# Kernel optimization log

Hardware: AMD Instinct MI355X
Metric: run time of the kernel (lower is better)

The kernel has to match this reference:

```python
import jax, jax.numpy as jnp
import numpy as np

N_NODES = 50000
N_EDGES = 800000
NUM_FEATURES = 128
H1, H2, H3 = 256, 512, 256


def setup_inputs() -> dict:
    key = jax.random.key(0)
    ks = jax.random.split(key, 14)

    def lin(kw, fan_in, fan_out):
        # torch nn.Linear-style init, stored as [in, out] for x @ W
        bound = 1.0 / np.sqrt(fan_in)
        W = jax.random.uniform(kw, (fan_in, fan_out), jnp.float32, -bound, bound)
        b = jnp.zeros((fan_out,), jnp.float32)
        return W, b

    x = jax.random.normal(ks[0], (N_NODES, NUM_FEATURES), jnp.float32)
    edge_index = jax.random.randint(ks[1], (2, N_EDGES), 0, N_NODES, jnp.int64 if jax.config.jax_enable_x64 else jnp.int32)

    W1, b1 = lin(ks[2], NUM_FEATURES, H1)
    W2, b2 = lin(ks[3], H1, H2)
    W3, b3 = lin(ks[4], H2, H3)
    Wf1, bf1 = lin(ks[5], H3, 128)
    Wf2, bf2 = lin(ks[6], 128, 64)
    Wf3, bf3 = lin(ks[7], 64, 1)

    return {"x": x, "edge_index": edge_index,
            "W1": W1, "b1": b1, "W2": W2, "b2": b2, "W3": W3, "b3": b3,
            "Wf1": Wf1, "bf1": bf1, "Wf2": Wf2, "bf2": bf2, "Wf3": Wf3, "bf3": bf3}


def gcn_conv(x, W, b, row, col, dinv_row_col, n):
    # PyG GCNConv: out = D^{-1/2} (A+I) D^{-1/2} (x W) + b, self-loops already in row/col
    h = x @ W                              # [N, out]
    msg = h[row] * dinv_row_col[:, None]   # gather + edge-wise scale: [E+N, out]
    return jax.ops.segment_sum(msg, col, num_segments=n) + b


def reference(x, edge_index, W1, b1, W2, b2, W3, b3, Wf1, bf1, Wf2, bf2, Wf3, bf3):
    n = x.shape[0]
    loop = jnp.arange(n, dtype=edge_index.dtype)
    row = jnp.concatenate([edge_index[0], loop])   # sources (with self-loops)
    col = jnp.concatenate([edge_index[1], loop])   # targets (with self-loops)

    # symmetric normalization (computed once; identical for all three convs)
    deg = jax.ops.segment_sum(jnp.ones(col.shape[0], x.dtype), col, num_segments=n)
    dinv = jnp.where(deg > 0, jax.lax.rsqrt(deg), 0.0)
    norm = dinv[row] * dinv[col]                   # [E+N]

    h = jax.nn.relu(gcn_conv(x, W1, b1, row, col, norm, n))
    h = jax.nn.relu(gcn_conv(h, W2, b2, row, col, norm, n))
    h = jax.nn.relu(gcn_conv(h, W3, b3, row, col, norm, n))

    g = jnp.mean(h, axis=0, keepdims=True)         # [1, H3]
    g = jax.nn.relu(g @ Wf1 + bf1)
    g = jax.nn.relu(g @ Wf2 + bf2)
    return g @ Wf3 + bf3                           # [1, 1]
```

## Files before the change

kernel.cpp:

```cpp
#include <hip/hip_runtime.h>
#include <hip/hip_bf16.h>

#define N_NODES 50000
#define N_EDGES 800000
#define N_BUCKETS 64
#define M_PAD 50048
#define SCAN_NB 196

typedef short short8 __attribute__((ext_vector_type(8)));
typedef float floatx4 __attribute__((ext_vector_type(4)));
typedef float floatx2 __attribute__((ext_vector_type(2)));

__device__ __forceinline__ unsigned short f2bf(float f) {
    unsigned u = __float_as_uint(f);
    unsigned r = (u + 0x7fff + ((u >> 16) & 1)) >> 16;
    return (unsigned short)r;
}
__device__ __forceinline__ float bf2f(unsigned short h) {
    return __uint_as_float(((unsigned)h) << 16);
}
__device__ __forceinline__ void expand2(unsigned u, float& lo, float& hi) {
    lo = __uint_as_float(u << 16);
    hi = __uint_as_float(u & 0xffff0000u);
}

__device__ __forceinline__ unsigned pack4_fp8(float f0, float f1, float f2, float f3) {
    int v = __builtin_amdgcn_cvt_pk_fp8_f32(f0, f1, 0, false);
    v = __builtin_amdgcn_cvt_pk_fp8_f32(f2, f3, v, true);
    return (unsigned)v;
}
__device__ __forceinline__ void accum_fp8x4(float* a, unsigned u, float w) {
    floatx2 lo = __builtin_amdgcn_cvt_pk_f32_fp8((int)u, false);
    floatx2 hi = __builtin_amdgcn_cvt_pk_f32_fp8((int)u, true);
    a[0] += lo[0] * w; a[1] += lo[1] * w;
    a[2] += hi[0] * w; a[3] += hi[1] * w;
}
__device__ __forceinline__ void accum_fp8x2(float* a, unsigned u, float w) {
    floatx2 lo = __builtin_amdgcn_cvt_pk_f32_fp8((int)u, false);
    a[0] += lo[0] * w; a[1] += lo[1] * w;
}

__device__ __forceinline__ void gload16(const void* gp, void* lp) {
    __builtin_amdgcn_global_load_lds(
        (const __attribute__((address_space(1))) unsigned int*)gp,
        (__attribute__((address_space(3))) unsigned int*)lp,
        16, 0, 0);
}

__global__ void k_init(int* __restrict__ cnt, float* __restrict__ gb) {
    int i = blockIdx.x * blockDim.x + threadIdx.x;
    if (i < N_NODES) cnt[i] = 0;
    if (i < N_BUCKETS * 256) gb[i] = 0.0f;
}

__global__ void k_count(const int* __restrict__ col, int* __restrict__ cnt) {
    int e = blockIdx.x * blockDim.x + threadIdx.x;
    if (e < N_EDGES) atomicAdd(&cnt[col[e]], 1);
}

__global__ __launch_bounds__(256) void k_scanA(const int* __restrict__ cnt,
                                               int* __restrict__ bsum) {
    __shared__ int red[256];
    int t = threadIdx.x;
    int i = blockIdx.x * 256 + t;
    red[t] = (i < N_NODES) ? ((cnt[i] + 1) & ~1) : 0;
    __syncthreads();
    for (int d = 128; d > 0; d >>= 1) {
        if (t < d) red[t] += red[t + d];
        __syncthreads();
    }
    if (t == 0) bsum[blockIdx.x] = red[0];
}

__global__ __launch_bounds__(256) void k_scanB(const int* __restrict__ bsum,
                                               int* __restrict__ bbase,
                                               int* __restrict__ off) {
    __shared__ int sc[256];
    int t = threadIdx.x;
    sc[t] = (t < SCAN_NB) ? bsum[t] : 0;
    __syncthreads();
    for (int d = 1; d < 256; d <<= 1) {
        int v = 0;
        if (t >= d) v = sc[t - d];
        __syncthreads();
        if (t >= d) sc[t] += v;
        __syncthreads();
    }
    if (t < SCAN_NB) bbase[t] = sc[t] - bsum[t];
    if (t == SCAN_NB - 1) off[N_NODES] = sc[t];
}

__global__ __launch_bounds__(256) void k_scanC(const int* __restrict__ cnt,
                                               const int* __restrict__ bbase,
                                               int* __restrict__ off,
                                               int* __restrict__ cursor,
                                               float* __restrict__ dinv,
                                               int2* __restrict__ epack) {
    __shared__ int sc[256];
    int t = threadIdx.x;
    int i = blockIdx.x * 256 + t;
    int c = (i < N_NODES) ? cnt[i] : 0;
    int cap = (c + 1) & ~1;
    sc[t] = cap;
    __syncthreads();
    for (int d = 1; d < 256; d <<= 1) {
        int v = 0;
        if (t >= d) v = sc[t - d];
        __syncthreads();
        if (t >= d) sc[t] += v;
        __syncthreads();
    }
    if (i < N_NODES) {
        int excl = sc[t] - cap + bbase[blockIdx.x];
        off[i] = excl;
        cursor[i] = excl;
        dinv[i] = 1.0f / sqrtf((float)(c + 1));
        if (c & 1) epack[excl + c] = make_int2(i, 0);
    }
}

__global__ void k_fill(const int* __restrict__ row, const int* __restrict__ col,
                       const float* __restrict__ dinv, int* __restrict__ cursor,
                       int2* __restrict__ epack) {
    int e = blockIdx.x * blockDim.x + threadIdx.x;
    if (e >= N_EDGES) return;
    int v = col[e];
    int p = atomicAdd(&cursor[v], 1);
    int r = row[e];
    epack[p] = make_int2(r, __float_as_int(dinv[r]));
}

__global__ void k_prepW(const float* __restrict__ W,
                        unsigned short* __restrict__ Th,
                        unsigned short* __restrict__ Tl, int K, int N) {
    int idx = blockIdx.x * blockDim.x + threadIdx.x;
    if (idx >= K * N) return;
    int n = idx / K, k = idx - n * K;
    float v = W[(size_t)k * N + n];
    unsigned short h = f2bf(v);
    Th[idx] = h;
    Tl[idx] = f2bf(v - bf2f(h));
}

__global__ void k_prepX8(const float* __restrict__ x, unsigned char* __restrict__ xq) {
    int i = blockIdx.x * blockDim.x + threadIdx.x;
    if (i >= N_NODES * 32) return;
    const float* s = x + (size_t)i * 4;
    *(unsigned*)&xq[(size_t)i * 4] = pack4_fp8(s[0], s[1], s[2], s[3]);
}

template <int DIM, int POOL>
__global__ __launch_bounds__(256) void k_aggf(
    const unsigned char* __restrict__ xq, const int* __restrict__ off,
    const int2* __restrict__ epack, const float* __restrict__ dinv,
    const float* __restrict__ bias, unsigned short* __restrict__ outb,
    float* __restrict__ gb) {
    const int FPL = DIM / 64;
    __shared__ float gpart[256];
    if (POOL) {
        gpart[threadIdx.x] = 0.0f;
        __syncthreads();
    }
    int wv = threadIdx.x >> 6;
    int li = threadIdx.x & 63;
    int v = blockIdx.x * 4 + wv;
    int f = li * FPL;
    float dv = dinv[v];
    const unsigned char* __restrict__ xf = xq + f;
    float a0[FPL], a1[FPL], a2[FPL], a3[FPL];
#pragma unroll
    for (int i = 0; i < FPL; ++i) { a0[i] = 0.f; a1[i] = 0.f; a2[i] = 0.f; a3[i] = 0.f; }
    if (FPL == 4) {
        accum_fp8x4(a0, *(const unsigned*)&xf[(size_t)v * DIM], dv);
    } else {
        accum_fp8x2(a0, (unsigned)*(const unsigned short*)&xf[(size_t)v * DIM], dv);
    }
    int s = off[v], e = off[v + 1];
    int j = s;
    for (; j + 4 <= e; j += 4) {
        int4 d0 = *(const int4*)&epack[j];
        int4 d1 = *(const int4*)&epack[j + 2];
        if (FPL == 4) {
            unsigned g0 = *(const unsigned*)&xf[(size_t)d0.x * DIM];
            unsigned g1 = *(const unsigned*)&xf[(size_t)d0.z * DIM];
            unsigned g2 = *(const unsigned*)&xf[(size_t)d1.x * DIM];
            unsigned g3 = *(const unsigned*)&xf[(size_t)d1.z * DIM];
            accum_fp8x4(a0, g0, __int_as_float(d0.y));
            accum_fp8x4(a1, g1, __int_as_float(d0.w));
            accum_fp8x4(a2, g2, __int_as_float(d1.y));
            accum_fp8x4(a3, g3, __int_as_float(d1.w));
        } else {
            unsigned g0 = *(const unsigned short*)&xf[(size_t)d0.x * DIM];
            unsigned g1 = *(const unsigned short*)&xf[(size_t)d0.z * DIM];
            unsigned g2 = *(const unsigned short*)&xf[(size_t)d1.x * DIM];
            unsigned g3 = *(const unsigned short*)&xf[(size_t)d1.z * DIM];
            accum_fp8x2(a0, g0, __int_as_float(d0.y));
            accum_fp8x2(a1, g1, __int_as_float(d0.w));
            accum_fp8x2(a2, g2, __int_as_float(d1.y));
            accum_fp8x2(a3, g3, __int_as_float(d1.w));
        }
    }
    if (j < e) {
        int4 d0 = *(const int4*)&epack[j];
        if (FPL == 4) {
            unsigned g0 = *(const unsigned*)&xf[(size_t)d0.x * DIM];
            unsigned g1 = *(const unsigned*)&xf[(size_t)d0.z * DIM];
            accum_fp8x4(a0, g0, __int_as_float(d0.y));
            accum_fp8x4(a1, g1, __int_as_float(d0.w));
        } else {
            unsigned g0 = *(const unsigned short*)&xf[(size_t)d0.x * DIM];
            unsigned g1 = *(const unsigned short*)&xf[(size_t)d0.z * DIM];
            accum_fp8x2(a0, g0, __int_as_float(d0.y));
            accum_fp8x2(a1, g1, __int_as_float(d0.w));
        }
    }
    float acc[FPL];
#pragma unroll
    for (int i = 0; i < FPL; ++i)
        acc[i] = ((a0[i] + a1[i]) + (a2[i] + a3[i])) * dv;
    if (!POOL) {
        if (FPL == 4) {
            uint2 o;
            o.x = (unsigned)f2bf(acc[0]) | ((unsigned)f2bf(acc[1]) << 16);
            o.y = (unsigned)f2bf(acc[2]) | ((unsigned)f2bf(acc[3]) << 16);
            *(uint2*)&outb[(size_t)v * DIM + f] = o;
        } else {
            unsigned o = (unsigned)f2bf(acc[0]) | ((unsigned)f2bf(acc[1]) << 16);
            *(unsigned*)&outb[(size_t)v * DIM + f] = o;
        }
    } else {
#pragma unroll
        for (int i = 0; i < FPL; ++i) {
            float r = fmaxf(acc[i] + bias[f + i], 0.0f);
            atomicAdd(&gpart[f + i], r);
        }
        __syncthreads();
        atomicAdd(&gb[(blockIdx.x & (N_BUCKETS - 1)) * 256 + threadIdx.x],
                  gpart[threadIdx.x]);
    }
}

template <int BIAS, int RELU, int OUTFP8>
__global__ __launch_bounds__(256) void k_gemm_b(
    const unsigned short* __restrict__ A,
    const unsigned short* __restrict__ Bh, const unsigned short* __restrict__ Bl,
    const float* __restrict__ bias, void* __restrict__ Cout,
    int M, int K, int N) {
    __shared__ unsigned short smem[4 * 4096];
    unsigned short* As  = smem;
    unsigned short* BsH = smem + 4096;
    unsigned short* BsL = smem + 8192;
    int tid = threadIdx.x;
    int lane = tid & 63;
    int w = tid >> 6;
    int wr = w & 1, wc = w >> 1;
    int bm = blockIdx.x * 128, bn = blockIdx.y * 128;

    floatx4 acc[4][4];
    floatx4 zero = {0.f, 0.f, 0.f, 0.f};
#pragma unroll
    for (int t = 0; t < 4; ++t)
#pragma unroll
        for (int u = 0; u < 4; ++u) acc[t][u] = zero;

    int c0 = w * 2, c1 = c0 + 1;
    int srow = lane >> 2;
    int kg = ((lane & 3) - ((lane >> 3) & 3)) & 3;
    int kc = kg * 8;
    const unsigned short* Ap0 = A + (size_t)(bm + c0 * 16 + srow) * K + kc;
    const unsigned short* Ap1 = A + (size_t)(bm + c1 * 16 + srow) * K + kc;
    const unsigned short* Bh0 = Bh + (size_t)(bn + c0 * 16 + srow) * K + kc;
    const unsigned short* Bh1 = Bh + (size_t)(bn + c1 * 16 + srow) * K + kc;
    const unsigned short* Bl0 = Bl + (size_t)(bn + c0 * 16 + srow) * K + kc;
    const unsigned short* Bl1 = Bl + (size_t)(bn + c1 * 16 + srow) * K + kc;

    const int KT = K >> 5;
    int fr = lane & 15;
    int fq = lane >> 4;
    int cl = ((fq + (fr >> 1)) & 3) * 8;

    for (int kt = 0; kt < KT; ++kt) {
        int k0 = kt * 32;
        gload16(Ap0 + k0, As + c0 * 512);
        gload16(Ap1 + k0, As + c1 * 512);
        gload16(Bh0 + k0, BsH + c0 * 512);
        gload16(Bh1 + k0, BsH + c1 * 512);
        gload16(Bl0 + k0, BsL + c0 * 512);
        gload16(Bl1 + k0, BsL + c1 * 512);
        __syncthreads();
        short8 av[4], bhv[4], blv[4];
#pragma unroll
        for (int t = 0; t < 4; ++t) {
            av[t]  = *(const short8*)&As[(wr * 64 + t * 16 + fr) * 32 + cl];
            bhv[t] = *(const short8*)&BsH[(wc * 64 + t * 16 + fr) * 32 + cl];
            blv[t] = *(const short8*)&BsL[(wc * 64 + t * 16 + fr) * 32 + cl];
        }
#pragma unroll
        for (int t = 0; t < 4; ++t)
#pragma unroll
            for (int u = 0; u < 4; ++u) {
                acc[t][u] = __builtin_amdgcn_mfma_f32_16x16x32_bf16(av[t], bhv[u], acc[t][u], 0, 0, 0);
                acc[t][u] = __builtin_amdgcn_mfma_f32_16x16x32_bf16(av[t], blv[u], acc[t][u], 0, 0, 0);
            }
        __syncthreads();
    }

    unsigned short* cq = smem + w * 4096;
#pragma unroll
    for (int u = 0; u < 4; ++u) {
        int colq = u * 16 + fr;
        float bv = BIAS ? bias[bn + wc * 64 + colq] : 0.0f;
#pragma unroll
        for (int t = 0; t < 4; ++t) {
#pragma unroll
            for (int r = 0; r < 4; ++r) {
                float o = acc[t][u][r] + bv;
                if (RELU) o = fmaxf(o, 0.f);
                cq[(t * 16 + fq * 4 + r) * 64 + colq] = f2bf(o);
            }
        }
    }
    __syncthreads();
    int lr = tid >> 4;
    int lc = (tid & 15) * 8;
    int wcq = lc >> 6;
    int lcq = lc & 63;
#pragma unroll
    for (int i = 0; i < 8; ++i) {
        int rowt = i * 16 + lr;
        int wrq = rowt >> 6;
        const unsigned short* src =
            smem + (wrq + wcq * 2) * 4096 + (rowt & 63) * 64 + lcq;
        int rowg = bm + rowt;
        if (rowg < M) {
            if (!OUTFP8) {
                unsigned short* C = (unsigned short*)Cout;
                *(uint4*)&C[(size_t)rowg * N + bn + lc] = *(const uint4*)src;
            } else {
                uint4 b = *(const uint4*)src;
                float f0, f1, f2, f3, f4, f5, f6, f7;
                expand2(b.x, f0, f1); expand2(b.y, f2, f3);
                expand2(b.z, f4, f5); expand2(b.w, f6, f7);
                uint2 q;
                q.x = pack4_fp8(f0, f1, f2, f3);
                q.y = pack4_fp8(f4, f5, f6, f7);
                unsigned char* C8 = (unsigned char*)Cout;
                *(uint2*)&C8[(size_t)rowg * N + bn + lc] = q;
            }
        }
    }
}

__global__ void k_mlp(const float* __restrict__ gb,
                      const float* __restrict__ Wf1, const float* __restrict__ bf1,
                      const float* __restrict__ Wf2, const float* __restrict__ bf2,
                      const float* __restrict__ Wf3, const float* __restrict__ bf3,
                      float* __restrict__ out) {
    __shared__ float s0[256], s1[128], s2[64];
    int t = threadIdx.x;
    float sum = 0.0f;
    for (int b = 0; b < N_BUCKETS; ++b) sum += gb[b * 256 + t];
    s0[t] = sum * (1.0f / (float)N_NODES);
    __syncthreads();
    if (t < 128) {
        float a = bf1[t];
        for (int k = 0; k < 256; ++k) a += s0[k] * Wf1[k * 128 + t];
        s1[t] = fmaxf(a, 0.0f);
    }
    __syncthreads();
    if (t < 64) {
        float a = bf2[t];
        for (int k = 0; k < 128; ++k) a += s1[k] * Wf2[k * 64 + t];
        s2[t] = fmaxf(a, 0.0f);
    }
    __syncthreads();
    if (t == 0) {
        float a = bf3[0];
        for (int k = 0; k < 64; ++k) a += s2[k] * Wf3[k];
        out[0] = a;
    }
}

extern "C" void kernel_launch(void* const* d_in, const int* in_sizes, int n_in,
                              void* d_out, int out_size, void* d_ws, size_t ws_size,
                              hipStream_t stream) {
    const float* x  = (const float*)d_in[0];
    const int* ei   = (const int*)d_in[1];
    const float* W1 = (const float*)d_in[2];
    const float* b1 = (const float*)d_in[3];
    const float* W2 = (const float*)d_in[4];
    const float* b2 = (const float*)d_in[5];
    const float* W3 = (const float*)d_in[6];
    const float* b3 = (const float*)d_in[7];
    const float* Wf1 = (const float*)d_in[8];
    const float* bf1 = (const float*)d_in[9];
    const float* Wf2 = (const float*)d_in[10];
    const float* bf2 = (const float*)d_in[11];
    const float* Wf3 = (const float*)d_in[12];
    const float* bf3 = (const float*)d_in[13];
    float* out = (float*)d_out;

    char* p = (char*)d_ws;
    auto alloc = [&](size_t bytes) {
        void* r = (void*)p;
        p += (bytes + 255) & ~((size_t)255);
        return r;
    };
    int*   cnt    = (int*)  alloc(N_NODES * sizeof(int));
    int*   off    = (int*)  alloc((N_NODES + 1) * sizeof(int));
    int*   cursor = (int*)  alloc(N_NODES * sizeof(int));
    int*   bsum   = (int*)  alloc(SCAN_NB * sizeof(int));
    int*   bbase  = (int*)  alloc(SCAN_NB * sizeof(int));
    float* dinv   = (float*)alloc(N_NODES * sizeof(float));
    int2*  epack  = (int2*) alloc((size_t)(N_EDGES + N_NODES) * sizeof(int2));
    float* gb     = (float*)alloc(N_BUCKETS * 256 * sizeof(float));
    unsigned short* W1h = (unsigned short*)alloc(128 * 256 * 2);
    unsigned short* W1l = (unsigned short*)alloc(128 * 256 * 2);
    unsigned short* W2h = (unsigned short*)alloc(256 * 512 * 2);
    unsigned short* W2l = (unsigned short*)alloc(256 * 512 * 2);
    unsigned short* W3h = (unsigned short*)alloc(512 * 256 * 2);
    unsigned short* W3l = (unsigned short*)alloc(512 * 256 * 2);
    unsigned char*  xq  = (unsigned char*) alloc((size_t)N_NODES * 128);
    unsigned short* t0  = (unsigned short*)alloc((size_t)M_PAD * 128 * 2);
    unsigned char*  h1q = (unsigned char*) alloc((size_t)N_NODES * 256);
    unsigned short* t1  = (unsigned short*)alloc((size_t)M_PAD * 256 * 2);
    unsigned short* h2  = (unsigned short*)alloc((size_t)M_PAD * 512 * 2);
    unsigned char*  t2q = (unsigned char*) alloc((size_t)N_NODES * 256);

    const int* row = ei;
    const int* col = ei + N_EDGES;

    const int NB = (N_NODES + 255) / 256;
    const int EB = (N_EDGES + 255) / 256;

    k_init<<<NB, 256, 0, stream>>>(cnt, gb);
    k_count<<<EB, 256, 0, stream>>>(col, cnt);
    k_scanA<<<SCAN_NB, 256, 0, stream>>>(cnt, bsum);
    k_scanB<<<1, 256, 0, stream>>>(bsum, bbase, off);
    k_scanC<<<SCAN_NB, 256, 0, stream>>>(cnt, bbase, off, cursor, dinv, epack);
    k_fill<<<EB, 256, 0, stream>>>(row, col, dinv, cursor, epack);

    k_prepW<<<(128 * 256 + 255) / 256, 256, 0, stream>>>(W1, W1h, W1l, 128, 256);
    k_prepW<<<(256 * 512 + 255) / 256, 256, 0, stream>>>(W2, W2h, W2l, 256, 512);
    k_prepW<<<(512 * 256 + 255) / 256, 256, 0, stream>>>(W3, W3h, W3l, 512, 256);
    k_prepX8<<<(N_NODES * 32 + 255) / 256, 256, 0, stream>>>(x, xq);

    const int M = N_NODES;
    const int MB = (M + 127) / 128;

    k_aggf<128, 0><<<N_NODES / 4, 256, 0, stream>>>(
        xq, off, epack, dinv, nullptr, t0, nullptr);
    {
        dim3 grid(MB, 256 / 128);
        k_gemm_b<1, 1, 1><<<grid, 256, 0, stream>>>(t0, W1h, W1l, b1, h1q, M, 128, 256);
    }
    k_aggf<256, 0><<<N_NODES / 4, 256, 0, stream>>>(
        h1q, off, epack, dinv, nullptr, t1, nullptr);
    {
        dim3 grid(MB, 512 / 128);
        k_gemm_b<1, 1, 0><<<grid, 256, 0, stream>>>(t1, W2h, W2l, b2, h2, M, 256, 512);
    }
    {
        dim3 grid(MB, 256 / 128);
        k_gemm_b<0, 0, 1><<<grid, 256, 0, stream>>>(h2, W3h, W3l, nullptr, t2q, M, 512, 256);
    }
    k_aggf<256, 1><<<N_NODES / 4, 256, 0, stream>>>(
        t2q, off, epack, dinv, b3, nullptr, gb);

    k_mlp<<<1, 256, 0, stream>>>(gb, Wf1, bf1, Wf2, bf2, Wf3, bf3, out);
}
```

Baseline: 456.0 us.

## Fold source-side dinv into producers and shrink edge list to int indices

Source-node normalization dinv[r] is now applied when features are produced (in the fp8 quantization of x and in the GEMM epilogues), so the aggregation kernels only sum gathered rows and apply the target dinv at the end. The edge list drops the per-edge weight and becomes a plain int array padded to multiples of 4, with pad slots pointing at a zeroed dummy row. The aggregation loop is unrolled by 8. This cuts edge-list bandwidth and per-edge multiplies, at the cost of extra padding gathers and quantizing pre-scaled values to fp8, which changes rounding.

```diff
diff --git a/kernel.cpp b/kernel.cpp
--- a/kernel.cpp
+++ b/kernel.cpp
@@ -6,6 +6,7 @@
 #define N_BUCKETS 64
 #define M_PAD 50048
 #define SCAN_NB 196
+#define ZROW N_NODES
 
 typedef short short8 __attribute__((ext_vector_type(8)));
 typedef float floatx4 __attribute__((ext_vector_type(4)));
@@ -29,15 +30,15 @@
     v = __builtin_amdgcn_cvt_pk_fp8_f32(f2, f3, v, true);
     return (unsigned)v;
 }
-__device__ __forceinline__ void accum_fp8x4(float* a, unsigned u, float w) {
+__device__ __forceinline__ void acc4(float* a, unsigned u) {
     floatx2 lo = __builtin_amdgcn_cvt_pk_f32_fp8((int)u, false);
     floatx2 hi = __builtin_amdgcn_cvt_pk_f32_fp8((int)u, true);
-    a[0] += lo[0] * w; a[1] += lo[1] * w;
-    a[2] += hi[0] * w; a[3] += hi[1] * w;
-}
-__device__ __forceinline__ void accum_fp8x2(float* a, unsigned u, float w) {
+    a[0] += lo[0]; a[1] += lo[1];
+    a[2] += hi[0]; a[3] += hi[1];
+}
+__device__ __forceinline__ void acc2(float* a, unsigned u) {
     floatx2 lo = __builtin_amdgcn_cvt_pk_f32_fp8((int)u, false);
-    a[0] += lo[0] * w; a[1] += lo[1] * w;
+    a[0] += lo[0]; a[1] += lo[1];
 }
 
 __device__ __forceinline__ void gload16(const void* gp, void* lp) {
@@ -47,10 +48,19 @@
         16, 0, 0);
 }
 
-__global__ void k_init(int* __restrict__ cnt, float* __restrict__ gb) {
+__global__ void k_init(int* __restrict__ cnt, float* __restrict__ gb,
+                       unsigned char* __restrict__ xq,
+                       unsigned char* __restrict__ h1q,
+                       unsigned char* __restrict__ t2q) {
     int i = blockIdx.x * blockDim.x + threadIdx.x;
     if (i < N_NODES) cnt[i] = 0;
     if (i < N_BUCKETS * 256) gb[i] = 0.0f;
+    if (blockIdx.x == 0) {
+        int t = threadIdx.x;
+        if (t < 32) ((unsigned*)(xq + (size_t)ZROW * 128))[t] = 0u;
+        if (t < 64) ((unsigned*)(h1q + (size_t)ZROW * 256))[t] = 0u;
+        if (t < 64) ((unsigned*)(t2q + (size_t)ZROW * 256))[t] = 0u;
+    }
 }
 
 __global__ void k_count(const int* __restrict__ col, int* __restrict__ cnt) {
@@ -63,7 +73,7 @@
     __shared__ int red[256];
     int t = threadIdx.x;
     int i = blockIdx.x * 256 + t;
-    red[t] = (i < N_NODES) ? ((cnt[i] + 1) & ~1) : 0;
+    red[t] = (i < N_NODES) ? ((cnt[i] + 4) & ~3) : 0;
     __syncthreads();
     for (int d = 128; d > 0; d >>= 1) {
         if (t < d) red[t] += red[t + d];
@@ -95,12 +105,12 @@
                                                int* __restrict__ off,
                                                int* __restrict__ cursor,
                                                float* __restrict__ dinv,
-                                               int2* __restrict__ epack) {
+                                               int* __restrict__ esrc) {
     __shared__ int sc[256];
     int t = threadIdx.x;
     int i = blockIdx.x * 256 + t;
     int c = (i < N_NODES) ? cnt[i] : 0;
-    int cap = (c + 1) & ~1;
+    int cap = (c + 4) & ~3;
     sc[t] = cap;
     __syncthreads();
     for (int d = 1; d < 256; d <<= 1) {
@@ -115,19 +125,17 @@
         off[i] = excl;
         cursor[i] = excl;
         dinv[i] = 1.0f / sqrtf((float)(c + 1));
-        if (c & 1) epack[excl + c] = make_int2(i, 0);
+        esrc[excl + c] = i;
+        for (int p = c + 1; p < cap; ++p) esrc[excl + p] = ZROW;
     }
 }
 
 __global__ void k_fill(const int* __restrict__ row, const int* __restrict__ col,
-                       const float* __restrict__ dinv, int* __restrict__ cursor,
-                       int2* __restrict__ epack) {
+                       int* __restrict__ cursor, int* __restrict__ esrc) {
     int e = blockIdx.x * blockDim.x + threadIdx.x;
     if (e >= N_EDGES) return;
-    int v = col[e];
-    int p = atomicAdd(&cursor[v], 1);
-    int r = row[e];
-    epack[p] = make_int2(r, __float_as_int(dinv[r]));
+    int p = atomicAdd(&cursor[col[e]], 1);
+    esrc[p] = row[e];
 }
 
 __global__ void k_prepW(const float* __restrict__ W,
@@ -142,22 +150,24 @@
     Tl[idx] = f2bf(v - bf2f(h));
 }
 
-__global__ void k_prepX8(const float* __restrict__ x, unsigned char* __restrict__ xq) {
+__global__ void k_prepX8(const float* __restrict__ x, const float* __restrict__ dinv,
+                         unsigned char* __restrict__ xq) {
     int i = blockIdx.x * blockDim.x + threadIdx.x;
     if (i >= N_NODES * 32) return;
+    float sc = dinv[i >> 5];
     const float* s = x + (size_t)i * 4;
-    *(unsigned*)&xq[(size_t)i * 4] = pack4_fp8(s[0], s[1], s[2], s[3]);
+    *(unsigned*)&xq[(size_t)i * 4] = pack4_fp8(s[0] * sc, s[1] * sc, s[2] * sc, s[3] * sc);
 }
 
 template <int DIM, int POOL>
-__global__ __launch_bounds__(256) void k_aggf(
+__global__ __launch_bounds__(256) void k_agg(
     const unsigned char* __restrict__ xq, const int* __restrict__ off,
-    const int2* __restrict__ epack, const float* __restrict__ dinv,
+    const int* __restrict__ esrc, const float* __restrict__ dinv,
     const float* __restrict__ bias, unsigned short* __restrict__ outb,
     float* __restrict__ gb) {
     const int FPL = DIM / 64;
     __shared__ float gpart[256];
-    if (POOL) {
+    if constexpr (POOL) {
         gpart[threadIdx.x] = 0.0f;
         __syncthreads();
     }
@@ -165,61 +175,59 @@
     int li = threadIdx.x & 63;
     int v = blockIdx.x * 4 + wv;
     int f = li * FPL;
-    float dv = dinv[v];
     const unsigned char* __restrict__ xf = xq + f;
     float a0[FPL], a1[FPL], a2[FPL], a3[FPL];
 #pragma unroll
     for (int i = 0; i < FPL; ++i) { a0[i] = 0.f; a1[i] = 0.f; a2[i] = 0.f; a3[i] = 0.f; }
-    if (FPL == 4) {
-        accum_fp8x4(a0, *(const unsigned*)&xf[(size_t)v * DIM], dv);
-    } else {
-        accum_fp8x2(a0, (unsigned)*(const unsigned short*)&xf[(size_t)v * DIM], dv);
-    }
-    int s = off[v], e = off[v + 1];
-    int j = s;
-    for (; j + 4 <= e; j += 4) {
-        int4 d0 = *(const int4*)&epack[j];
-        int4 d1 = *(const int4*)&epack[j + 2];
-        if (FPL == 4) {
-            unsigned g0 = *(const unsigned*)&xf[(size_t)d0.x * DIM];
-            unsigned g1 = *(const unsigned*)&xf[(size_t)d0.z * DIM];
-            unsigned g2 = *(const unsigned*)&xf[(size_t)d1.x * DIM];
-            unsigned g3 = *(const unsigned*)&xf[(size_t)d1.z * DIM];
-            accum_fp8x4(a0, g0, __int_as_float(d0.y));
-            accum_fp8x4(a1, g1, __int_as_float(d0.w));
-            accum_fp8x4(a2, g2, __int_as_float(d1.y));
-            accum_fp8x4(a3, g3, __int_as_float(d1.w));
+    int j = off[v], e = off[v + 1];
+    for (; j + 8 <= e; j += 8) {
+        int4 dA = *(const int4*)&esrc[j];
+        int4 dB = *(const int4*)&esrc[j + 4];
+        if constexpr (DIM == 256) {
+            unsigned g0 = *(const unsigned*)&xf[(size_t)dA.x * DIM];
+            unsigned g1 = *(const unsigned*)&xf[(size_t)dA.y * DIM];
+            unsigned g2 = *(const unsigned*)&xf[(size_t)dA.z * DIM];
+            unsigned g3 = *(const unsigned*)&xf[(size_t)dA.w * DIM];
+            unsigned g4 = *(const unsigned*)&xf[(size_t)dB.x * DIM];
+            unsigned g5 = *(const unsigned*)&xf[(size_t)dB.y * DIM];
+            unsigned g6 = *(const unsigned*)&xf[(size_t)dB.z * DIM];
+            unsigned g7 = *(const unsigned*)&xf[(size_t)dB.w * DIM];
+            acc4(a0, g0); acc4(a1, g1); acc4(a2, g2); acc4(a3, g3);
+            acc4(a0, g4); acc4(a1, g5); acc4(a2, g6); acc4(a3, g7);
         } else {
-            unsigned g0 = *(const unsigned short*)&xf[(size_t)d0.x * DIM];
-            unsigned g1 = *(const unsigned short*)&xf[(size_t)d0.z * DIM];
-            unsigned g2 = *(const unsigned short*)&xf[(size_t)d1.x * DIM];
-            unsigned g3 = *(const unsigned short*)&xf[(size_t)d1.z * DIM];
-            accum_fp8x2(a0, g0, __int_as_float(d0.y));
-            accum_fp8x2(a1, g1, __int_as_float(d0.w));
-            accum_fp8x2(a2, g2, __int_as_float(d1.y));
-            accum_fp8x2(a3, g3, __int_as_float(d1.w));
+            unsigned g0 = *(const unsigned short*)&xf[(size_t)dA.x * DIM];
+            unsigned g1 = *(const unsigned short*)&xf[(size_t)dA.y * DIM];
+            unsigned g2 = *(const unsigned short*)&xf[(size_t)dA.z * DIM];
+            unsigned g3 = *(const unsigned short*)&xf[(size_t)dA.w * DIM];
+            unsigned g4 = *(const unsigned short*)&xf[(size_t)dB.x * DIM];
+            unsigned g5 = *(const unsigned short*)&xf[(size_t)dB.y * DIM];
+            unsigned g6 = *(const unsigned short*)&xf[(size_t)dB.z * DIM];
+            unsigned g7 = *(const unsigned short*)&xf[(size_t)dB.w * DIM];
+            acc2(a0, g0); acc2(a1, g1); acc2(a2, g2); acc2(a3, g3);
+            acc2(a0, g4); acc2(a1, g5); acc2(a2, g6); acc2(a3, g7);
         }
     }
     if (j < e) {
-        int4 d0 = *(const int4*)&epack[j];
-        if (FPL == 4) {
-            unsigned g0 = *(const unsigned*)&xf[(size_t)d0.x * DIM];
-            unsigned g1 = *(const unsigned*)&xf[(size_t)d0.z * DIM];
-            accum_fp8x4(a0, g0, __int_as_float(d0.y));
-            accum_fp8x4(a1, g1, __int_as_float(d0.w));
+        int4 dA = *(const int4*)&esrc[j];
+        if constexpr (DIM == 256) {
+            acc4(a0, *(const unsigned*)&xf[(size_t)dA.x * DIM]);
+            acc4(a1, *(const unsigned*)&xf[(size_t)dA.y * DIM]);
+            acc4(a2, *(const unsigned*)&xf[(size_t)dA.z * DIM]);
+            acc4(a3, *(const unsigned*)&xf[(size_t)dA.w * DIM]);
         } else {
-            unsigned g0 = *(const unsigned short*)&xf[(size_t)d0.x * DIM];
-            unsigned g1 = *(const unsigned short*)&xf[(size_t)d0.z * DIM];
-            accum_fp8x2(a0, g0, __int_as_float(d0.y));
-            accum_fp8x2(a1, g1, __int_as_float(d0.w));
-        }
-    }
+            acc2(a0, *(const unsigned short*)&xf[(size_t)dA.x * DIM]);
+            acc2(a1, *(const unsigned short*)&xf[(size_t)dA.y * DIM]);
+            acc2(a2, *(const unsigned short*)&xf[(size_t)dA.z * DIM]);
+            acc2(a3, *(const unsigned short*)&xf[(size_t)dA.w * DIM]);
+        }
+    }
+    float dv = dinv[v];
     float acc[FPL];
 #pragma unroll
     for (int i = 0; i < FPL; ++i)
         acc[i] = ((a0[i] + a1[i]) + (a2[i] + a3[i])) * dv;
-    if (!POOL) {
-        if (FPL == 4) {
+    if constexpr (!POOL) {
+        if constexpr (DIM == 256) {
             uint2 o;
             o.x = (unsigned)f2bf(acc[0]) | ((unsigned)f2bf(acc[1]) << 16);
             o.y = (unsigned)f2bf(acc[2]) | ((unsigned)f2bf(acc[3]) << 16);
@@ -240,12 +248,12 @@
     }
 }
 
-template <int BIAS, int RELU, int OUTFP8>
+template <int BIAS, int RELU, int OUTFP8, int DVSCALE>
 __global__ __launch_bounds__(256) void k_gemm_b(
     const unsigned short* __restrict__ A,
     const unsigned short* __restrict__ Bh, const unsigned short* __restrict__ Bl,
-    const float* __restrict__ bias, void* __restrict__ Cout,
-    int M, int K, int N) {
+    const float* __restrict__ bias, const float* __restrict__ dinv,
+    void* __restrict__ Cout, int M, int K, int N) {
     __shared__ unsigned short smem[4 * 4096];
     unsigned short* As  = smem;
     unsigned short* BsH = smem + 4096;
@@ -337,13 +345,14 @@
                 unsigned short* C = (unsigned short*)Cout;
                 *(uint4*)&C[(size_t)rowg * N + bn + lc] = *(const uint4*)src;
             } else {
+                float sc = DVSCALE ? dinv[rowg] : 1.0f;
                 uint4 b = *(const uint4*)src;
                 float f0, f1, f2, f3, f4, f5, f6, f7;
                 expand2(b.x, f0, f1); expand2(b.y, f2, f3);
                 expand2(b.z, f4, f5); expand2(b.w, f6, f7);
                 uint2 q;
-                q.x = pack4_fp8(f0, f1, f2, f3);
-                q.y = pack4_fp8(f4, f5, f6, f7);
+                q.x = pack4_fp8(f0 * sc, f1 * sc, f2 * sc, f3 * sc);
+                q.y = pack4_fp8(f4 * sc, f5 * sc, f6 * sc, f7 * sc);
                 unsigned char* C8 = (unsigned char*)Cout;
                 *(uint2*)&C8[(size_t)rowg * N + bn + lc] = q;
             }
@@ -412,7 +421,7 @@
     int*   bsum   = (int*)  alloc(SCAN_NB * sizeof(int));
     int*   bbase  = (int*)  alloc(SCAN_NB * sizeof(int));
     float* dinv   = (float*)alloc(N_NODES * sizeof(float));
-    int2*  epack  = (int2*) alloc((size_t)(N_EDGES + N_NODES) * sizeof(int2));
+    int*   esrc   = (int*)  alloc((size_t)(N_EDGES + 4 * N_NODES) * sizeof(int));
     float* gb     = (float*)alloc(N_BUCKETS * 256 * sizeof(float));
     unsigned short* W1h = (unsigned short*)alloc(128 * 256 * 2);
     unsigned short* W1l = (unsigned short*)alloc(128 * 256 * 2);
@@ -420,12 +429,12 @@
     unsigned short* W2l = (unsigned short*)alloc(256 * 512 * 2);
     unsigned short* W3h = (unsigned short*)alloc(512 * 256 * 2);
     unsigned short* W3l = (unsigned short*)alloc(512 * 256 * 2);
-    unsigned char*  xq  = (unsigned char*) alloc((size_t)N_NODES * 128);
+    unsigned char*  xq  = (unsigned char*) alloc((size_t)(N_NODES + 1) * 128);
     unsigned short* t0  = (unsigned short*)alloc((size_t)M_PAD * 128 * 2);
-    unsigned char*  h1q = (unsigned char*) alloc((size_t)N_NODES * 256);
+    unsigned char*  h1q = (unsigned char*) alloc((size_t)(N_NODES + 1) * 256);
     unsigned short* t1  = (unsigned short*)alloc((size_t)M_PAD * 256 * 2);
     unsigned short* h2  = (unsigned short*)alloc((size_t)M_PAD * 512 * 2);
-    unsigned char*  t2q = (unsigned char*) alloc((size_t)N_NODES * 256);
+    unsigned char*  t2q = (unsigned char*) alloc((size_t)(N_NODES + 1) * 256);
 
     const int* row = ei;
     const int* col = ei + N_EDGES;
@@ -433,39 +442,39 @@
     const int NB = (N_NODES + 255) / 256;
     const int EB = (N_EDGES + 255) / 256;
 
-    k_init<<<NB, 256, 0, stream>>>(cnt, gb);
+    k_init<<<NB, 256, 0, stream>>>(cnt, gb, xq, h1q, t2q);
     k_count<<<EB, 256, 0, stream>>>(col, cnt);
     k_scanA<<<SCAN_NB, 256, 0, stream>>>(cnt, bsum);
     k_scanB<<<1, 256, 0, stream>>>(bsum, bbase, off);
-    k_scanC<<<SCAN_NB, 256, 0, stream>>>(cnt, bbase, off, cursor, dinv, epack);
-    k_fill<<<EB, 256, 0, stream>>>(row, col, dinv, cursor, epack);
+    k_scanC<<<SCAN_NB, 256, 0, stream>>>(cnt, bbase, off, cursor, dinv, esrc);
+    k_fill<<<EB, 256, 0, stream>>>(row, col, cursor, esrc);
 
     k_prepW<<<(128 * 256 + 255) / 256, 256, 0, stream>>>(W1, W1h, W1l, 128, 256);
     k_prepW<<<(256 * 512 + 255) / 256, 256, 0, stream>>>(W2, W2h, W2l, 256, 512);
     k_prepW<<<(512 * 256 + 255) / 256, 256, 0, stream>>>(W3, W3h, W3l, 512, 256);
-    k_prepX8<<<(N_NODES * 32 + 255) / 256, 256, 0, stream>>>(x, xq);
+    k_prepX8<<<(N_NODES * 32 + 255) / 256, 256, 0, stream>>>(x, dinv, xq);
 
     const int M = N_NODES;
     const int MB = (M + 127) / 128;
 
-    k_aggf<128, 0><<<N_NODES / 4, 256, 0, stream>>>(
-        xq, off, epack, dinv, nullptr, t0, nullptr);
+    k_agg<128, 0><<<N_NODES / 4, 256, 0, stream>>>(
+        xq, off, esrc, dinv, nullptr, t0, nullptr);
     {
         dim3 grid(MB, 256 / 128);
-        k_gemm_b<1, 1, 1><<<grid, 256, 0, stream>>>(t0, W1h, W1l, b1, h1q, M, 128, 256);
-    }
-    k_aggf<256, 0><<<N_NODES / 4, 256, 0, stream>>>(
-        h1q, off, epack, dinv, nullptr, t1, nullptr);
+        k_gemm_b<1, 1, 1, 1><<<grid, 256, 0, stream>>>(t0, W1h, W1l, b1, dinv, h1q, M, 128, 256);
+    }
+    k_agg<256, 0><<<N_NODES / 4, 256, 0, stream>>>(
+        h1q, off, esrc, dinv, nullptr, t1, nullptr);
     {
         dim3 grid(MB, 512 / 128);
-        k_gemm_b<1, 1, 0><<<grid, 256, 0, stream>>>(t1, W2h, W2l, b2, h2, M, 256, 512);
+        k_gemm_b<1, 1, 0, 0><<<grid, 256, 0, stream>>>(t1, W2h, W2l, b2, nullptr, h2, M, 256, 512);
     }
     {
         dim3 grid(MB, 256 / 128);
-        k_gemm_b<0, 0, 1><<<grid, 256, 0, stream>>>(h2, W3h, W3l, nullptr, t2q, M, 512, 256);
-    }
-    k_aggf<256, 1><<<N_NODES / 4, 256, 0, stream>>>(
-        t2q, off, epack, dinv, b3, nullptr, gb);
+        k_gemm_b<0, 0, 1, 1><<<grid, 256, 0, stream>>>(h2, W3h, W3l, nullptr, dinv, t2q, M, 512, 256);
+    }
+    k_agg<256, 1><<<N_NODES / 4, 256, 0, stream>>>(
+        t2q, off, esrc, dinv, b3, nullptr, gb);
 
     k_mlp<<<1, 256, 0, stream>>>(gb, Wf1, bf1, Wf2, bf2, Wf3, bf3, out);
 }
```

Result: no change. 461.9 us (+1.3%).
